# Kernel tuning notes

Hardware: AMD Instinct MI355X
Metric: run time of the kernel (lower is better)

## Reference

```python
import jax, jax.numpy as jnp
import numpy as np

D_MODEL = 1024
HEAD_DIM = 64

def setup_inputs() -> dict:
    key = jax.random.key(0)
    ks = jax.random.split(key, 7)
    x = jax.random.normal(ks[0], (4, 4096, D_MODEL), dtype=jnp.float32)
    s = 1.0 / np.sqrt(D_MODEL)
    Wq = jax.random.uniform(ks[1], (D_MODEL, HEAD_DIM), jnp.float32, -s, s)
    bq = jax.random.uniform(ks[2], (HEAD_DIM,), jnp.float32, -s, s)
    Wk = jax.random.uniform(ks[3], (D_MODEL, HEAD_DIM), jnp.float32, -s, s)
    bk = jax.random.uniform(ks[4], (HEAD_DIM,), jnp.float32, -s, s)
    Wv = jax.random.uniform(ks[5], (D_MODEL, HEAD_DIM), jnp.float32, -s, s)
    bv = jax.random.uniform(ks[6], (HEAD_DIM,), jnp.float32, -s, s)
    return {"x": x, "Wq": Wq, "bq": bq, "Wk": Wk, "bk": bk, "Wv": Wv, "bv": bv}

def reference(x, Wq, bq, Wk, bk, Wv, bv):
    B, T, _ = x.shape
    q = x @ Wq + bq  # [B, T, H]
    k = x @ Wk + bk
    v = x @ Wv + bv
    scale = 1.0 / jnp.sqrt(jnp.asarray(q.shape[-1], q.dtype))
    scores = jnp.einsum('bqh,bkh->bqk', q, k) * scale  # [B, T, T]
    causal = jnp.tril(jnp.ones((T, T), dtype=bool))
    scores = jnp.where(causal, scores, jnp.asarray(-jnp.inf, scores.dtype))
    attn = jax.nn.softmax(scores, axis=-1)
    return jnp.einsum('bqk,bkh->bqh', attn, v)
```

## Files before the change

kernel.cpp:

```cpp
#include <hip/hip_runtime.h>

#define BATCH 4
#define SEQ 4096
#define DMODEL 1024
#define HDIM 64

#define QBLK 64
#define NQT 64
#define CHUNK 256
#define ITERS 8
#define BSLOT 544
#define MAXC 17

typedef _Float16 h16;
typedef _Float16 h16x8 __attribute__((ext_vector_type(8)));
typedef _Float16 h16x4 __attribute__((ext_vector_type(4)));
typedef float f32x4 __attribute__((ext_vector_type(4)));
typedef float f32x16 __attribute__((ext_vector_type(16)));

#define WF_ELEMS (12 * 32 * 64 * 8)
#define QK_ELEMS (BATCH * SEQ * HDIM)
#define PB 262144
#define NSLOT (BATCH * BSLOT)

__device__ __forceinline__ int slot_base(int qt) {
    int a = qt >> 2, b = qt & 3;
    return (a + 1) * (2 * a + b);
}

__device__ __forceinline__ int kperm(int u) {
    return (u & 3) | (((u >> 2) & 1) << 3) | (((u >> 3) & 1) << 2);
}

template<int OFF>
__device__ __forceinline__ void gload_o(h16x8& dst, const h16* p) {
    asm volatile("global_load_dwordx4 %0, %1, off offset:%2" : "=v"(dst) : "v"(p), "n"(OFF));
}

__global__ __launch_bounds__(256) void prep(const float* __restrict__ Wq,
                                            const float* __restrict__ Wk,
                                            const float* __restrict__ Wv,
                                            const float* __restrict__ x,
                                            h16* __restrict__ Wf,
                                            h16* __restrict__ xh) {
    int b = blockIdx.x;
    if (b < 96) {
        int flat = b * 256 + threadIdx.x;
        int lane = flat & 63;
        int kt = (flat >> 6) & 31;
        int fg = flat >> 11;
        int col = 16 * fg + (lane & 15);
        const float* W = (col < 64) ? Wq : (col < 128) ? Wk : Wv;
        int c = col & 63;
        int k0 = 32 * kt + 8 * (lane >> 4);
        h16x8 v;
        #pragma unroll
        for (int j = 0; j < 8; j++) v[j] = (h16)W[(size_t)(k0 + j) * 64 + c];
        *(h16x8*)(Wf + (size_t)flat * 8) = v;
        return;
    }
    size_t flat = (size_t)(b - 96) * 256 + threadIdx.x;
    int lane = (int)(flat & 63);
    int kt = (int)((flat >> 6) & 31);
    int mt = (int)(flat >> 11);
    const float* xp = x + (size_t)(16 * mt + (lane & 15)) * DMODEL + 32 * kt + 8 * (lane >> 4);
    f32x4 lo = *(const f32x4*)xp;
    f32x4 hi = *(const f32x4*)(xp + 4);
    h16x8 v;
    #pragma unroll
    for (int j = 0; j < 4; j++) { v[j] = (h16)lo[j]; v[j + 4] = (h16)hi[j]; }
    *(h16x8*)(xh + flat * 8) = v;
}

#define QISSUE(S, IMM)                                                        \
    gload_o<IMM>(a##S##0, ax0); gload_o<IMM>(a##S##1, ax1);                   \
    gload_o<IMM>(b##S##0, w0);  gload_o<IMM>(b##S##1, w1);                    \
    gload_o<IMM>(b##S##2, w2);

#define QCOMPUTE(S)                                                           \
    c00 = __builtin_amdgcn_mfma_f32_16x16x32_f16(a##S##0, b##S##0, c00, 0, 0, 0); \
    c01 = __builtin_amdgcn_mfma_f32_16x16x32_f16(a##S##0, b##S##1, c01, 0, 0, 0); \
    c02 = __builtin_amdgcn_mfma_f32_16x16x32_f16(a##S##0, b##S##2, c02, 0, 0, 0); \
    c10 = __builtin_amdgcn_mfma_f32_16x16x32_f16(a##S##1, b##S##0, c10, 0, 0, 0); \
    c11 = __builtin_amdgcn_mfma_f32_16x16x32_f16(a##S##1, b##S##1, c11, 0, 0, 0); \
    c12 = __builtin_amdgcn_mfma_f32_16x16x32_f16(a##S##1, b##S##2, c12, 0, 0, 0);

#define QSTEP(S, N) {                                                         \
    asm volatile("s_waitcnt vmcnt(" #N ")" ::: "memory");                     \
    __builtin_amdgcn_sched_barrier(0);                                        \
    QCOMPUTE(S)                                                               \
    QISSUE(S, 3072)                                                           \
    ax0 += 512; ax1 += 512; w0 += 512; w1 += 512; w2 += 512; }

#define QSTEP_T(S, N) {                                                       \
    asm volatile("s_waitcnt vmcnt(" #N ")" ::: "memory");                     \
    __builtin_amdgcn_sched_barrier(0);                                        \
    QCOMPUTE(S) }

__global__ __launch_bounds__(256, 2) void qkv_proj(
    const h16* __restrict__ xh, const h16* __restrict__ Wf,
    const float* __restrict__ bq, const float* __restrict__ bk, const float* __restrict__ bv,
    h16* __restrict__ Qf, h16* __restrict__ Kf, h16* __restrict__ Vf)
{
    int lane = threadIdx.x & 63;
    int w = threadIdx.x >> 6;
    int r0 = blockIdx.x * 32;
    int ln15 = lane & 15;

    const h16* ax0 = xh + (size_t)(2 * blockIdx.x) * 16384 + lane * 8 + 512;
    const h16* ax1 = ax0 + 16384;
    const h16* w0 = Wf + (size_t)(3 * w) * 16384 + lane * 8 + 512;
    const h16* w1 = w0 + 16384;
    const h16* w2 = w0 + 32768;

    h16x8 aA0, aA1, bA0, bA1, bA2;
    h16x8 aB0, aB1, bB0, bB1, bB2;
    h16x8 aC0, aC1, bC0, bC1, bC2;
    h16x8 aD0, aD1, bD0, bD1, bD2;
    f32x4 c00 = {}, c01 = {}, c02 = {}, c10 = {}, c11 = {}, c12 = {};

    QISSUE(A, -1024) QISSUE(B, 0) QISSUE(C, 1024) QISSUE(D, 2048)

    QSTEP(A, 15) QSTEP(B, 15) QSTEP(C, 15) QSTEP(D, 15)
    QSTEP(A, 15) QSTEP(B, 15) QSTEP(C, 15) QSTEP(D, 15)
    QSTEP(A, 15) QSTEP(B, 15) QSTEP(C, 15) QSTEP(D, 15)
    QSTEP(A, 15) QSTEP(B, 15) QSTEP(C, 15) QSTEP(D, 15)
    QSTEP(A, 15) QSTEP(B, 15) QSTEP(C, 15) QSTEP(D, 15)
    QSTEP(A, 15) QSTEP(B, 15) QSTEP(C, 15) QSTEP(D, 15)
    QSTEP(A, 15) QSTEP(B, 15) QSTEP(C, 15) QSTEP(D, 15)
    QSTEP_T(A, 15) QSTEP_T(B, 10) QSTEP_T(C, 5) QSTEP_T(D, 0)

    f32x4 acc[2][3] = {{c00, c01, c02}, {c10, c11, c12}};
    #pragma unroll
    for (int f = 0; f < 3; f++) {
        int col = 48 * w + 16 * f + ln15;
        float bias = (col < 64) ? bq[col] : (col < 128) ? bk[col - 64] : bv[col - 128];
        #pragma unroll
        for (int m = 0; m < 2; m++) {
            #pragma unroll
            for (int i = 0; i < 4; i++) {
                int t = r0 + 16 * m + (lane >> 4) * 4 + i;
                int bb = t >> 12;
                int tt = t & (SEQ - 1);
                float v = acc[m][f][i] + bias;
                if (col < 64) {
                    int d = col >> 4, hh = (col >> 3) & 1, e = col & 7;
                    Qf[(size_t)bb * PB + (tt >> 5) * 2048 + d * 512 +
                       (hh * 32 + (tt & 31)) * 8 + e] = (h16)(v * 0.125f);
                } else if (col < 128) {
                    int ck = col - 64;
                    int d = ck >> 4, hh = (ck >> 3) & 1, e = ck & 7;
                    Kf[(size_t)bb * PB + (tt >> 5) * 2048 + d * 512 +
                       (hh * 32 + (tt & 31)) * 8 + e] = (h16)v;
                } else {
                    int h = col - 128;
                    int tp = (tt & ~15) | kperm(tt & 15);
                    int j = ((h >> 5) << 1) | ((tp >> 4) & 1);
                    Vf[(size_t)bb * PB + (tp >> 5) * 2048 + j * 512 +
                       (((tp >> 3) & 1) * 32 + (h & 31)) * 8 + (tp & 7)] = (h16)v;
                }
            }
        }
    }
}

__device__ __forceinline__ void flash_compute(
    h16x8 K0, h16x8 K1, h16x8 K2, h16x8 K3,
    h16x8 V0, h16x8 V1, h16x8 V2, h16x8 V3,
    h16x8 q0v, h16x8 q1v, h16x8 q2v, h16x8 q3v,
    int kt0, int q0g, int qg, int hi,
    f32x16& o0, f32x16& o1, float& m_i, float& l_i)
{
    f32x16 s = {};
    s = __builtin_amdgcn_mfma_f32_32x32x16_f16(K0, q0v, s, 0, 0, 0);
    s = __builtin_amdgcn_mfma_f32_32x32x16_f16(K1, q1v, s, 0, 0, 0);
    s = __builtin_amdgcn_mfma_f32_32x32x16_f16(K2, q2v, s, 0, 0, 0);
    s = __builtin_amdgcn_mfma_f32_32x32x16_f16(K3, q3v, s, 0, 0, 0);

    float sc[16];
    #pragma unroll
    for (int r = 0; r < 16; r++) sc[r] = s[r];
    if (kt0 + 31 > q0g) {
        #pragma unroll
        for (int r = 0; r < 16; r++) {
            int kg = kt0 + (r & 3) + 8 * (r >> 2) + 4 * hi;
            if (kg > qg) sc[r] = -1e30f;
        }
    }
    float tm = sc[0];
    #pragma unroll
    for (int r = 1; r < 16; r++) tm = fmaxf(tm, sc[r]);
    tm = fmaxf(tm, __shfl_xor(tm, 32));
    float mn = fmaxf(m_i, tm);
    float al = __expf(m_i - mn);
    m_i = mn;
    float p[16], rs = 0.f;
    #pragma unroll
    for (int r = 0; r < 16; r++) { p[r] = __expf(sc[r] - mn); rs += p[r]; }
    rs += __shfl_xor(rs, 32);
    l_i = l_i * al + rs;
    #pragma unroll
    for (int r = 0; r < 16; r++) { o0[r] *= al; o1[r] *= al; }

    h16x8 pb0, pb1;
    #pragma unroll
    for (int j = 0; j < 8; j++) { pb0[j] = (h16)p[j]; pb1[j] = (h16)p[8 + j]; }

    o0 = __builtin_amdgcn_mfma_f32_32x32x16_f16(V0, pb0, o0, 0, 0, 0);
    o0 = __builtin_amdgcn_mfma_f32_32x32x16_f16(V1, pb1, o0, 0, 0, 0);
    o1 = __builtin_amdgcn_mfma_f32_32x32x16_f16(V2, pb0, o1, 0, 0, 0);
    o1 = __builtin_amdgcn_mfma_f32_32x32x16_f16(V3, pb1, o1, 0, 0, 0);
}

#define ISSUE(B) {                                                            \
    gload_o<0>(k##B##0, kp);    gload_o<1024>(k##B##1, kp);                   \
    gload_o<2048>(k##B##2, kp); gload_o<3072>(k##B##3, kp);                   \
    gload_o<0>(v##B##0, vp);    gload_o<1024>(v##B##1, vp);                   \
    gload_o<2048>(v##B##2, vp); gload_o<3072>(v##B##3, vp);                   \
    kp += 2048; vp += 2048; }

#define COMPUTE(B, T) {                                                       \
    __builtin_amdgcn_s_setprio(1);                                            \
    flash_compute(k##B##0, k##B##1, k##B##2, k##B##3,                         \
                  v##B##0, v##B##1, v##B##2, v##B##3,                         \
                  qa0, qa1, qa2, qa3, S + 32 * (T), q0, qg0, hi,              \
                  o00, o01, m0, l0);                                          \
    flash_compute(k##B##0, k##B##1, k##B##2, k##B##3,                         \
                  v##B##0, v##B##1, v##B##2, v##B##3,                         \
                  qc0, qc1, qc2, qc3, S + 32 * (T), q0 + 32, qg1, hi,         \
                  o10, o11, m1, l1);                                          \
    __builtin_amdgcn_s_setprio(0); }

#define STEP(CUR, NXT, T) {                                                   \
    ISSUE(NXT)                                                                \
    asm volatile("s_waitcnt vmcnt(8)" ::: "memory");                          \
    __builtin_amdgcn_sched_barrier(0);                                        \
    COMPUTE(CUR, T) }

#define STEP_LAST(CUR, T) {                                                   \
    asm volatile("s_waitcnt vmcnt(0)" ::: "memory");                          \
    __builtin_amdgcn_sched_barrier(0);                                        \
    COMPUTE(CUR, T) }

__global__ __launch_bounds__(256, 2) void flash(
    const h16* __restrict__ Qf, const h16* __restrict__ Kf, const h16* __restrict__ Vf,
    h16* __restrict__ o_part, float* __restrict__ ml_part)
{
    int wid = threadIdx.x >> 6;
    int lane = threadIdx.x & 63;
    int bid = blockIdx.x;
    int quarter = bid % 5;
    int rest = bid / 5;
    int qtflip = rest & (NQT - 1);
    int batch = rest >> 6;
    int qt = NQT - 1 - qtflip;
    int c = quarter * 4 + wid;
    int nc = (qt >> 2) + 1;
    if (c >= nc) return;

    int q0 = qt * QBLK;
    int S = c * CHUNK;
    int l31 = lane & 31;
    int hi = lane >> 5;
    int qg0 = q0 + l31;
    int qg1 = q0 + 32 + l31;

    const h16* kp = Kf + (size_t)batch * PB + (S >> 5) * 2048 + lane * 8;
    const h16* vp = Vf + (size_t)batch * PB + (S >> 5) * 2048 + lane * 8;

    h16x8 qa0, qa1, qa2, qa3, qc0, qc1, qc2, qc3;
    {
        const h16* qp = Qf + (size_t)batch * PB + (q0 >> 5) * 2048 + lane * 8;
        gload_o<0>(qa0, qp); gload_o<1024>(qa1, qp);
        gload_o<2048>(qa2, qp); gload_o<3072>(qa3, qp);
        const h16* qp2 = qp + 2048;
        gload_o<0>(qc0, qp2); gload_o<1024>(qc1, qp2);
        gload_o<2048>(qc2, qp2); gload_o<3072>(qc3, qp2);
    }

    h16x8 kA0, kA1, kA2, kA3, vA0, vA1, vA2, vA3;
    h16x8 kB0, kB1, kB2, kB3, vB0, vB1, vB2, vB3;

    f32x16 o00 = {}, o01 = {}, o10 = {}, o11 = {};
    float m0 = -1e30f, l0 = 0.f, m1 = -1e30f, l1 = 0.f;

    ISSUE(A)

    STEP(A, B, 0)
    STEP(B, A, 1)
    STEP(A, B, 2)
    STEP(B, A, 3)
    STEP(A, B, 4)
    STEP(B, A, 5)
    STEP(A, B, 6)
    STEP_LAST(B, 7)

    size_t slot = (size_t)batch * BSLOT + slot_base(qt) + c;
    h16* opb = o_part + slot * (QBLK * 64);
    {
        float inv = 1.f / l0;
        h16* op = opb + l31 * 64;
        #pragma unroll
        for (int q = 0; q < 4; q++) {
            h16x4 pk0, pk1;
            #pragma unroll
            for (int i = 0; i < 4; i++) {
                pk0[i] = (h16)(o00[4 * q + i] * inv);
                pk1[i] = (h16)(o01[4 * q + i] * inv);
            }
            *(h16x4*)(op + 8 * q + 4 * hi) = pk0;
            *(h16x4*)(op + 32 + 8 * q + 4 * hi) = pk1;
        }
    }
    {
        float inv = 1.f / l1;
        h16* op = opb + (32 + l31) * 64;
        #pragma unroll
        for (int q = 0; q < 4; q++) {
            h16x4 pk0, pk1;
            #pragma unroll
            for (int i = 0; i < 4; i++) {
                pk0[i] = (h16)(o10[4 * q + i] * inv);
                pk1[i] = (h16)(o11[4 * q + i] * inv);
            }
            *(h16x4*)(op + 8 * q + 4 * hi) = pk0;
            *(h16x4*)(op + 32 + 8 * q + 4 * hi) = pk1;
        }
    }
    if (hi == 0) {
        ml_part[slot * 128 + l31 * 2] = m0;
        ml_part[slot * 128 + l31 * 2 + 1] = l0;
        ml_part[slot * 128 + (32 + l31) * 2] = m1;
        ml_part[slot * 128 + (32 + l31) * 2 + 1] = l1;
    }
}

__global__ __launch_bounds__(256) void combine(
    const h16* __restrict__ o_part, const float* __restrict__ ml_part,
    float* __restrict__ out)
{
    __shared__ float mlds[MAXC * 128];
    int bid = blockIdx.x;
    int rq = bid & 3;
    int tile = bid >> 2;
    int batch = tile >> 6;
    int qt = tile & (NQT - 1);
    int q0 = qt * QBLK;
    int nc = (qt >> 2) + 1;
    size_t base = (size_t)batch * BSLOT + slot_base(qt);

    for (int i = threadIdx.x; i < nc * 128; i += 256)
        mlds[i] = ml_part[base * 128 + i];
    __syncthreads();

    int col = threadIdx.x & 63;
    int rg = threadIdx.x >> 6;
    int r0 = rq * 16 + rg * 4;
    const h16* op = o_part + base * (QBLK * 64) + (size_t)r0 * 64 + col;

    float M[4];
    #pragma unroll
    for (int j = 0; j < 4; j++) {
        float m = -1e30f;
        for (int c = 0; c < nc; c++) m = fmaxf(m, mlds[c * 128 + (r0 + j) * 2]);
        M[j] = m;
    }

    float L4[4] = {0.f, 0.f, 0.f, 0.f}, A4[4] = {0.f, 0.f, 0.f, 0.f};
    #pragma unroll 2
    for (int c = 0; c < nc; c++) {
        #pragma unroll
        for (int j = 0; j < 4; j++) {
            float wt = __expf(mlds[c * 128 + (r0 + j) * 2] - M[j]) *
                       mlds[c * 128 + (r0 + j) * 2 + 1];
            L4[j] += wt;
            A4[j] += wt * (float)op[(size_t)c * (QBLK * 64) + j * 64];
        }
    }
    #pragma unroll
    for (int j = 0; j < 4; j++)
        out[((size_t)batch * SEQ + q0 + r0 + j) * HDIM + col] = A4[j] / L4[j];
}

extern "C" void kernel_launch(void* const* d_in, const int* in_sizes, int n_in,
                              void* d_out, int out_size, void* d_ws, size_t ws_size,
                              hipStream_t stream) {
    const float* x  = (const float*)d_in[0];
    const float* Wq = (const float*)d_in[1];
    const float* bq = (const float*)d_in[2];
    const float* Wk = (const float*)d_in[3];
    const float* bk = (const float*)d_in[4];
    const float* Wv = (const float*)d_in[5];
    const float* bv = (const float*)d_in[6];
    float* out = (float*)d_out;

    h16* Wf = (h16*)d_ws;
    h16* Qf = Wf + WF_ELEMS;
    h16* Kf = Qf + QK_ELEMS;
    h16* Vf = Kf + QK_ELEMS;
    h16* xh = Vf + QK_ELEMS;
    h16* o_part = xh;
    float* ml_part = (float*)(o_part + (size_t)NSLOT * QBLK * 64);

    hipLaunchKernelGGL(prep, dim3(96 + 8192), dim3(256), 0, stream, Wq, Wk, Wv, x, Wf, xh);
    hipLaunchKernelGGL(qkv_proj, dim3(512), dim3(256), 0, stream,
                       xh, Wf, bq, bk, bv, Qf, Kf, Vf);
    hipLaunchKernelGGL(flash, dim3(BATCH * NQT * 5), dim3(256), 0, stream,
                       Qf, Kf, Vf, o_part, ml_part);
    hipLaunchKernelGGL(combine, dim3(BATCH * NQT * 4), dim3(256), 0, stream,
                       o_part, ml_part, out);
}
```

Before: 74.88 us.

## Fold log2e into Q scale, use lazy softmax rescaling, vectorize combine

```diff
diff --git a/kernel.cpp b/kernel.cpp
--- a/kernel.cpp
+++ b/kernel.cpp
@@ -11,6 +11,8 @@
 #define ITERS 8
 #define BSLOT 544
 #define MAXC 17
+
+#define QSCALE 0.18033688f
 
 typedef _Float16 h16;
 typedef _Float16 h16x8 __attribute__((ext_vector_type(8)));
@@ -146,7 +148,7 @@
                 if (col < 64) {
                     int d = col >> 4, hh = (col >> 3) & 1, e = col & 7;
                     Qf[(size_t)bb * PB + (tt >> 5) * 2048 + d * 512 +
-                       (hh * 32 + (tt & 31)) * 8 + e] = (h16)(v * 0.125f);
+                       (hh * 32 + (tt & 31)) * 8 + e] = (h16)(v * QSCALE);
                 } else if (col < 128) {
                     int ck = col - 64;
                     int d = ck >> 4, hh = (ck >> 3) & 1, e = ck & 7;
@@ -191,16 +193,21 @@
     #pragma unroll
     for (int r = 1; r < 16; r++) tm = fmaxf(tm, sc[r]);
     tm = fmaxf(tm, __shfl_xor(tm, 32));
-    float mn = fmaxf(m_i, tm);
-    float al = __expf(m_i - mn);
-    m_i = mn;
+
+    if (!__all(tm - m_i <= 8.f)) {
+        float mn = fmaxf(m_i, tm);
+        float al = exp2f(m_i - mn);
+        m_i = mn;
+        l_i *= al;
+        #pragma unroll
+        for (int r = 0; r < 16; r++) { o0[r] *= al; o1[r] *= al; }
+    }
+
     float p[16], rs = 0.f;
     #pragma unroll
-    for (int r = 0; r < 16; r++) { p[r] = __expf(sc[r] - mn); rs += p[r]; }
+    for (int r = 0; r < 16; r++) { p[r] = exp2f(sc[r] - m_i); rs += p[r]; }
     rs += __shfl_xor(rs, 32);
-    l_i = l_i * al + rs;
-    #pragma unroll
-    for (int r = 0; r < 16; r++) { o0[r] *= al; o1[r] *= al; }
+    l_i += rs;
 
     h16x8 pb0, pb1;
     #pragma unroll
@@ -353,33 +360,30 @@
         mlds[i] = ml_part[base * 128 + i];
     __syncthreads();
 
-    int col = threadIdx.x & 63;
-    int rg = threadIdx.x >> 6;
-    int r0 = rq * 16 + rg * 4;
-    const h16* op = o_part + base * (QBLK * 64) + (size_t)r0 * 64 + col;
-
-    float M[4];
-    #pragma unroll
-    for (int j = 0; j < 4; j++) {
-        float m = -1e30f;
-        for (int c = 0; c < nc; c++) m = fmaxf(m, mlds[c * 128 + (r0 + j) * 2]);
-        M[j] = m;
-    }
-
-    float L4[4] = {0.f, 0.f, 0.f, 0.f}, A4[4] = {0.f, 0.f, 0.f, 0.f};
-    #pragma unroll 2
+    int r = rq * 16 + (threadIdx.x >> 4);
+    int c4 = (threadIdx.x & 15) * 4;
+
+    float M = -1e30f;
+    for (int c = 0; c < nc; c++) M = fmaxf(M, mlds[c * 128 + r * 2]);
+
+    const h16* op = o_part + base * (QBLK * 64) + r * 64 + c4;
+    float L = 0.f;
+    f32x4 A = {};
+    #pragma unroll 4
     for (int c = 0; c < nc; c++) {
-        #pragma unroll
-        for (int j = 0; j < 4; j++) {
-            float wt = __expf(mlds[c * 128 + (r0 + j) * 2] - M[j]) *
-                       mlds[c * 128 + (r0 + j) * 2 + 1];
-            L4[j] += wt;
-            A4[j] += wt * (float)op[(size_t)c * (QBLK * 64) + j * 64];
-        }
-    }
-    #pragma unroll
-    for (int j = 0; j < 4; j++)
-        out[((size_t)batch * SEQ + q0 + r0 + j) * HDIM + col] = A4[j] / L4[j];
+        float wt = exp2f(mlds[c * 128 + r * 2] - M) * mlds[c * 128 + r * 2 + 1];
+        L += wt;
+        h16x4 v = *(const h16x4*)(op + (size_t)c * (QBLK * 64));
+        A[0] += wt * (float)v[0];
+        A[1] += wt * (float)v[1];
+        A[2] += wt * (float)v[2];
+        A[3] += wt * (float)v[3];
+    }
+    f32x4 o;
+    float inv = 1.f / L;
+    #pragma unroll
+    for (int j = 0; j < 4; j++) o[j] = A[j] * inv;
+    *(f32x4*)(out + ((size_t)batch * SEQ + q0 + r) * HDIM + c4) = o;
 }
 
 extern "C" void kernel_launch(void* const* d_in, const int* in_sizes, int n_in,
```

After: 73.87 us. Within noise of the previous version (-1.3%).
